# Optimization experiments

Hardware: AMD Instinct MI355X
Metric: run time of the kernel (lower is better)

The kernel has to match this reference:

```python
import jax, jax.numpy as jnp
import numpy as np
import math

DIM = 768
EMB = 768          # dim * num_heads (num_heads=1)
NBLOCKS = 4
M = EMB // 2       # kernel_ratio = 0.5 -> 384 random features
EPS = 1e-8


def monarch_linear(x, w1, w2, b):
    """Monarch (blockdiag butterfly) linear: x [..., n] -> [..., out].
    w1: (k, q, p) with n = k*p ; w2: (l, s, r) with k*q = l*r ; out = l*s."""
    lead = x.shape[:-1]
    k, q, p = w1.shape
    l, s, r = w2.shape
    xf = x.reshape(-1, k, p)                              # (B, k, p)
    o1 = jnp.einsum('bkp,kqp->bkq', xf, w1)               # (B, k, q)
    o1 = o1.transpose(0, 2, 1).reshape(-1, l, r)          # permute then (B, l, r)
    o2 = jnp.einsum('blr,lsr->bls', o1, w2)               # (B, l, s)
    out = o2.transpose(0, 2, 1).reshape(*lead, s * l)     # (B, s, l) flattened
    return out + b


def prm_exp(x, w):
    """FAVOR+ positive random features. x: [b,t,d], w: [m,d]."""
    xd = 0.5 * jnp.sum(x * x, axis=-1, keepdims=True)     # [b,t,1]
    wtx = jnp.einsum('btd,md->btm', x, w)                 # [b,t,m]
    return jnp.exp(wtx - xd) / math.sqrt(M)


def _monarch_params(rng, n_in, n_out, nblocks):
    in_blk = n_in // nblocks
    out_blk = n_out // nblocks
    if n_in < n_out:
        w1 = rng.standard_normal((nblocks, in_blk, in_blk)).astype(np.float32)
        w2 = rng.standard_normal((nblocks, out_blk, in_blk)).astype(np.float32)
    else:
        w1 = rng.standard_normal((nblocks, out_blk, in_blk)).astype(np.float32)
        w2 = rng.standard_normal((nblocks, out_blk, out_blk)).astype(np.float32)
    scale = 1.0 / math.sqrt(n_in)
    b = rng.standard_normal((n_out,)).astype(np.float32) * scale
    return w1 * scale, w2 * scale, b


def setup_inputs() -> dict:
    key = jax.random.key(0)
    x = jax.random.normal(key, (8, 4096, DIM), dtype=jnp.float32)
    rng = np.random.default_rng(0)
    kqv_w1, kqv_w2, kqv_b = _monarch_params(rng, DIM, 3 * EMB, NBLOCKS)
    proj_w1, proj_w2, proj_b = _monarch_params(rng, EMB, EMB, NBLOCKS)
    # orthogonal random-feature matrix, rows orthonormal, scaled by sqrt(m)
    a = rng.standard_normal((EMB, M)).astype(np.float64)
    qmat, _ = np.linalg.qr(a)                             # (EMB, M), cols orthonormal
    w = (qmat.T * math.sqrt(M)).astype(np.float32)        # (M, EMB)
    return {
        'x': x,
        'kqv_w1': jnp.asarray(kqv_w1), 'kqv_w2': jnp.asarray(kqv_w2), 'kqv_b': jnp.asarray(kqv_b),
        'proj_w1': jnp.asarray(proj_w1), 'proj_w2': jnp.asarray(proj_w2), 'proj_b': jnp.asarray(proj_b),
        'w': jnp.asarray(w),
    }


def reference(x, kqv_w1, kqv_w2, kqv_b, proj_w1, proj_w2, proj_b, w):
    kqv = monarch_linear(x, kqv_w1, kqv_w2, kqv_b)        # [b,t,3*EMB]
    k, q, v = jnp.split(kqv, 3, axis=-1)                  # order k,q,v as in torch.split
    kp = prm_exp(k, w)                                    # [b,t,m]
    qp = prm_exp(q, w)                                    # [b,t,m]
    D = jnp.einsum('btm,bm->bt', qp, kp.sum(axis=1))[:, :, None]   # [b,t,1]
    kptv = jnp.einsum('btn,btm->bnm', v, kp)              # [b,EMB,m]
    y = jnp.einsum('btm,bnm->btn', qp, kptv) / (D + EPS)  # [b,t,EMB]
    return monarch_linear(y, proj_w1, proj_w2, proj_b)
```

## Files before the change

### kernel.cpp

```cpp
#include <hip/hip_runtime.h>


#define NTOK   32768
#define RSQRTM 0.05103103630798288f

typedef _Float16 f16;
typedef f16   f16x8 __attribute__((ext_vector_type(8)));
typedef f16   f16x4 __attribute__((ext_vector_type(4)));
typedef short s16x8 __attribute__((ext_vector_type(8)));
typedef float f32x4 __attribute__((ext_vector_type(4)));

typedef const void __attribute__((address_space(1))) gv_t;
typedef void       __attribute__((address_space(3))) lv_t;
#define GLL16(g, l) __builtin_amdgcn_global_load_lds((gv_t*)(g), (lv_t*)(l), 16, 0, 0)

__device__ __forceinline__ float b2f(unsigned short u){
  union{unsigned int i; float f;} v; v.i = ((unsigned int)u)<<16; return v.f;
}
__device__ __forceinline__ unsigned short f2b(float f){
  union{float f; unsigned int i;} v; v.f = f;
  unsigned int x = v.i;
  x += 0x7fffu + ((x>>16)&1u);
  return (unsigned short)(x>>16);
}

template<typename T> struct MfmaOp;
template<> struct MfmaOp<f16> {
  typedef f16x8 frag;
  static __device__ __forceinline__ f32x4 run(frag a, frag b, f32x4 c){
    return __builtin_amdgcn_mfma_f32_16x16x32_f16(a, b, c, 0, 0, 0);
  }
};
template<> struct MfmaOp<short> {
  typedef s16x8 frag;
  static __device__ __forceinline__ f32x4 run(frag a, frag b, f32x4 c){
    return __builtin_amdgcn_mfma_f32_16x16x32_bf16(a, b, c, 0, 0, 0);
  }
};

__global__ void cvt16(const float4* __restrict__ src, f16* __restrict__ dst, int n4){
  const int i = blockIdx.x*256 + threadIdx.x;
  if (i >= n4) return;
  const float4 v = src[i];
  f16x4 h; h[0]=(f16)v.x; h[1]=(f16)v.y; h[2]=(f16)v.z; h[3]=(f16)v.w;
  *reinterpret_cast<f16x4*>(dst + 4*(long)i) = h;
}
__global__ void build_wkqvT(const float* __restrict__ w1, const float* __restrict__ w2,
                            f16* __restrict__ Wt){
  const int idx = blockIdx.x*256 + threadIdx.x;
  const int j = idx / 768, i = idx % 768;
  const int k = i / 192, p = i % 192;
  const int s = j >> 2,  l = j & 3;
  float acc = 0.f;
  #pragma unroll 4
  for(int u=0; u<48; ++u)
    acc += w1[(k*192 + l*48+u)*192 + p] * w2[(l*576+s)*192 + 4*u+k];
  Wt[idx] = (f16)acc;
}
__global__ void build_wprojT(const float* __restrict__ w1, const float* __restrict__ w2,
                             unsigned short* __restrict__ Wt){
  const int idx = blockIdx.x*256 + threadIdx.x;
  const int j = idx / 768, i = idx % 768;
  const int k = i / 192, p = i % 192;
  const int s = j >> 2,  l = j & 3;
  float acc = 0.f;
  #pragma unroll 4
  for(int u=0; u<48; ++u)
    acc += w1[(k*192 + l*48+u)*192 + p] * w2[(l*192+s)*192 + 4*u+k];
  Wt[idx] = f2b(acc);
}
__global__ void reduce_kptv(const float* __restrict__ p32, unsigned short* __restrict__ o){
  const int idx = blockIdx.x*256 + threadIdx.x;
  const int b = idx / 294912, i = idx % 294912;
  const float* base = p32 + (long)b*4*294912 + i;
  o[idx] = f2b(base[0] + base[294912] + base[2*294912] + base[3*294912]);
}

template<typename T, int BM, int BN, int EPI, int SPLIT>
__global__ __launch_bounds__(256)
void mgemm(const T* __restrict__ A, int lda, long aB,
           const T* __restrict__ Bt, int ldb, long bB,
           int K, void* __restrict__ out, int ldo, long outB,
           void* __restrict__ out2,
           const float* __restrict__ aux, long auxB,
           float* __restrict__ aux2){
  constexpr int MT = BM/32, NT = BN/32;
  constexpr int IA = BM/32, IB = BN/32;
  __shared__ T As[BM*64];
  __shared__ T Bs[BN*64];
  typedef typename MfmaOp<T>::frag frag_t;

  const int tid = threadIdx.x, lane = tid & 63, w = tid >> 6;
  const int wm = w >> 1, wn = w & 1;
  const int ln = lane & 15, q = lane >> 4;
  const int bz = blockIdx.z;
  const int batch = bz / SPLIT;
  const int kstart = (bz % SPLIT) * K;
  const long m0 = (long)blockIdx.y * BM;
  const int  n0 = blockIdx.x * BN;
  const T* Ab = A  + (long)batch*aB;
  const T* Bb = Bt + (long)batch*bB;

  f32x4 acc[MT][NT];
  const f32x4 zero = {0.f, 0.f, 0.f, 0.f};
  #pragma unroll
  for(int i=0;i<MT;i++)
    #pragma unroll
    for(int j=0;j<NT;j++) acc[i][j] = zero;

  for (int k0 = kstart; k0 < kstart + K; k0 += 64){
    __syncthreads();
    #pragma unroll
    for (int i = 0; i < IA; ++i){
      const int e = (w*IA + i)*64 + lane;
      const int m = e >> 3, j = (e & 7) ^ (m & 7);
      GLL16(Ab + (m0 + m)*lda + k0 + j*8, As + (size_t)(w*IA + i)*512);
    }
    #pragma unroll
    for (int i = 0; i < IB; ++i){
      const int e = (w*IB + i)*64 + lane;
      const int n = e >> 3, j = (e & 7) ^ (n & 7);
      GLL16(Bb + (long)(n0 + n)*ldb + k0 + j*8, Bs + (size_t)(w*IB + i)*512);
    }
    __syncthreads();

    #pragma unroll
    for (int kk = 0; kk < 2; ++kk){
      frag_t a[MT], b[NT];
      #pragma unroll
      for (int mt=0; mt<MT; ++mt){
        const int r = wm*MT*16 + mt*16 + ln;
        a[mt] = *reinterpret_cast<const frag_t*>(&As[(r*8 + ((kk*4+q) ^ (r&7)))*8]);
      }
      #pragma unroll
      for (int nt=0; nt<NT; ++nt){
        const int r = wn*NT*16 + nt*16 + ln;
        b[nt] = *reinterpret_cast<const frag_t*>(&Bs[(r*8 + ((kk*4+q) ^ (r&7)))*8]);
      }
      #pragma unroll
      for (int mt=0; mt<MT; ++mt)
        #pragma unroll
        for (int nt=0; nt<NT; ++nt)
          acc[mt][nt] = MfmaOp<T>::run(a[mt], b[nt], acc[mt][nt]);
    }
  }

  if constexpr(EPI==1){
    const int b = (int)(m0 >> 12);
    float cs[NT];
    #pragma unroll
    for(int nt=0;nt<NT;nt++) cs[nt]=0.f;
    #pragma unroll
    for (int mt=0; mt<MT; ++mt){
      const long mbase = m0 + wm*MT*16 + mt*16 + q*4;
      float xv[4];
      #pragma unroll
      for(int r=0;r<4;r++) xv[r] = aux[mbase + r];
      #pragma unroll
      for (int nt=0; nt<NT; ++nt){
        const int n = n0 + wn*NT*16 + nt*16 + ln;
        const f32x4 c = acc[mt][nt];
        ushort4 v;
        v.x = f2b(__expf(c[0]-xv[0])*RSQRTM);
        v.y = f2b(__expf(c[1]-xv[1])*RSQRTM);
        v.z = f2b(__expf(c[2]-xv[2])*RSQRTM);
        v.w = f2b(__expf(c[3]-xv[3])*RSQRTM);
        *reinterpret_cast<ushort4*>(&((unsigned short*)out)[(long)n*ldo + mbase]) = v;
        cs[nt] += b2f(v.x)+b2f(v.y)+b2f(v.z)+b2f(v.w);
      }
    }
    #pragma unroll
    for (int nt=0; nt<NT; ++nt){
      cs[nt] += __shfl_xor(cs[nt], 16);
      cs[nt] += __shfl_xor(cs[nt], 32);
      if (lane < 16)
        atomicAdd(&aux2[b*384 + n0 + wn*NT*16 + nt*16 + lane], cs[nt]);
    }
    return;
  }

  #pragma unroll
  for (int mt=0; mt<MT; ++mt){
    const long mbase = m0 + wm*MT*16 + mt*16 + q*4;
    if constexpr(EPI==0){
      const int nw = n0 + wn*NT*16;
      const int part = nw / 768;
      float p[4] = {0.f,0.f,0.f,0.f};
      #pragma unroll
      for (int nt=0; nt<NT; ++nt){
        const int n = nw + nt*16 + ln;
        const f32x4 c = acc[mt][nt];
        const float bv = aux[n];
        if (part < 2){
          f16* KQ = (f16*)out;
          #pragma unroll
          for(int r=0;r<4;r++){
            const f16 h = (f16)(c[r] + bv);
            KQ[(mbase+r)*1536 + n] = h;
            const float hf = (float)h;
            p[r] += hf*hf;
          }
        } else {
          unsigned short* VT = (unsigned short*)out2;
          ushort4 v;
          v.x = f2b(c[0]+bv); v.y = f2b(c[1]+bv); v.z = f2b(c[2]+bv); v.w = f2b(c[3]+bv);
          *reinterpret_cast<ushort4*>(&VT[(long)(n-1536)*32768 + mbase]) = v;
        }
      }
      if (part < 2){
        #pragma unroll
        for(int r=0;r<4;r++){
          #pragma unroll
          for(int mask=1; mask<16; mask<<=1) p[r] += __shfl_xor(p[r], mask);
        }
        if (ln == 0){
          #pragma unroll
          for(int r=0;r<4;r++)
            atomicAdd(&aux2[part*NTOK + mbase + r], 0.5f*p[r]);
        }
      }
    } else if constexpr(EPI==2){
      const int b = (int)(m0 >> 12);
      float xv[4], dp[4] = {0.f,0.f,0.f,0.f};
      #pragma unroll
      for(int r=0;r<4;r++) xv[r] = aux[mbase + r];
      #pragma unroll
      for (int nt=0; nt<NT; ++nt){
        const int n = n0 + wn*NT*16 + nt*16 + ln;
        const f32x4 c = acc[mt][nt];
        const float ksn = aux2[b*384 + n];
        #pragma unroll
        for(int r=0;r<4;r++){
          const unsigned short h = f2b(__expf(c[r]-xv[r])*RSQRTM);
          ((unsigned short*)out)[(mbase+r)*ldo + n] = h;
          dp[r] += b2f(h)*ksn;
        }
      }
      #pragma unroll
      for(int r=0;r<4;r++){
        #pragma unroll
        for(int mask=1; mask<16; mask<<=1) dp[r] += __shfl_xor(dp[r], mask);
      }
      if (ln == 0){
        #pragma unroll
        for(int r=0;r<4;r++)
          atomicAdd(&((float*)out2)[mbase + r], dp[r]);
      }
    } else if constexpr(EPI==3){
      float* o = (float*)out + (long)bz*outB;
      #pragma unroll
      for (int nt=0; nt<NT; ++nt){
        const int n = n0 + wn*NT*16 + nt*16 + ln;
        const f32x4 c = acc[mt][nt];
        #pragma unroll
        for(int r=0;r<4;r++) o[(mbase+r)*ldo + n] = c[r];
      }
    } else if constexpr(EPI==4){
      unsigned short* o = (unsigned short*)out + (long)bz*outB;
      float xv[4];
      #pragma unroll
      for(int r=0;r<4;r++) xv[r] = 1.f/(aux[bz*auxB + mbase + r] + 1e-8f);
      #pragma unroll
      for (int nt=0; nt<NT; ++nt){
        const int n = n0 + wn*NT*16 + nt*16 + ln;
        const f32x4 c = acc[mt][nt];
        #pragma unroll
        for(int r=0;r<4;r++) o[(mbase+r)*ldo + n] = f2b(c[r]*xv[r]);
      }
    } else if constexpr(EPI==5){
      float* o = (float*)out;
      #pragma unroll
      for (int nt=0; nt<NT; ++nt){
        const int n = n0 + wn*NT*16 + nt*16 + ln;
        const f32x4 c = acc[mt][nt];
        const float bv = aux[n];
        #pragma unroll
        for(int r=0;r<4;r++) o[(mbase+r)*ldo + n] = c[r] + bv;
      }
    }
  }
}

extern "C" void kernel_launch(void* const* d_in, const int* in_sizes, int n_in,
                              void* d_out, int out_size, void* d_ws, size_t ws_size,
                              hipStream_t stream){
  (void)in_sizes; (void)n_in; (void)out_size;
  const float* x       = (const float*)d_in[0];
  const float* kqv_w1  = (const float*)d_in[1];
  const float* kqv_w2  = (const float*)d_in[2];
  const float* kqv_b   = (const float*)d_in[3];
  const float* proj_w1 = (const float*)d_in[4];
  const float* proj_w2 = (const float*)d_in[5];
  const float* proj_b  = (const float*)d_in[6];
  const float* w       = (const float*)d_in[7];
  char* ws = (char*)d_ws;

  const size_t o_WkqvT  = 0;
  const size_t o_WprojT = 3538944;
  const size_t o_w16    = 4718592;
  const size_t o_x16    = 5308416;
  const size_t o_KQ     = 55640064;
  const size_t o_VT     = 156303360;
  const size_t o_xd     = 206635008;
  const size_t o_ksum   = 206897152;
  const size_t o_Dv     = 206909440;
  const size_t o_kpT    = 207040512;
  const size_t o_qp     = 232206336;
  const size_t o_kptv32 = 257372160;
  const size_t o_kptv   = 295120896;
  const size_t o_Y      = 299839488;
  const size_t TOTAL    = 350171136;
  if (ws_size < TOTAL) return;

  f16*            WkqvT  = (f16*)(ws + o_WkqvT);
  short*          WprojT = (short*)(ws + o_WprojT);
  f16*            w16    = (f16*)(ws + o_w16);
  f16*            x16    = (f16*)(ws + o_x16);
  f16*            KQ     = (f16*)(ws + o_KQ);
  short*          VT     = (short*)(ws + o_VT);
  float*          xd     = (float*)(ws + o_xd);
  float*          ksum   = (float*)(ws + o_ksum);
  float*          Dv     = (float*)(ws + o_Dv);
  short*          kpT    = (short*)(ws + o_kpT);
  short*          qp     = (short*)(ws + o_qp);
  float*          kptv32 = (float*)(ws + o_kptv32);
  unsigned short* kptv   = (unsigned short*)(ws + o_kptv);
  short*          Y      = (short*)(ws + o_Y);

  hipMemsetAsync(ws + o_xd, 0, 405504, stream);

  cvt16<<<24576, 256, 0, stream>>>((const float4*)x, x16, 6291456);
  cvt16<<<288,   256, 0, stream>>>((const float4*)w, w16, 73728);
  build_wkqvT <<<6912, 256, 0, stream>>>(kqv_w1, kqv_w2, WkqvT);
  build_wprojT<<<2304, 256, 0, stream>>>(proj_w1, proj_w2, (unsigned short*)WprojT);

  mgemm<f16,128,128,0,1><<<dim3(18,256,1), 256, 0, stream>>>(
      x16, 768, 0L, WkqvT, 768, 0L, 768, KQ, 1536, 0L, VT, kqv_b, 0L, xd);

  mgemm<f16,128,128,1,1><<<dim3(3,256,1), 256, 0, stream>>>(
      KQ, 1536, 0L, w16, 768, 0L, 768, kpT, 32768, 0L, nullptr, xd, 0L, ksum);

  mgemm<f16,128,128,2,1><<<dim3(3,256,1), 256, 0, stream>>>(
      KQ + 768, 1536, 0L, w16, 768, 0L, 768, qp, 384, 0L, Dv, xd + NTOK, 0L, ksum);

  mgemm<short,128,128,3,4><<<dim3(3,6,32), 256, 0, stream>>>(
      VT, 32768, 4096L, kpT, 32768, 4096L, 1024, kptv32, 384, 294912L,
      nullptr, nullptr, 0L, nullptr);
  reduce_kptv<<<9216, 256, 0, stream>>>(kptv32, kptv);

  mgemm<short,128,128,4,1><<<dim3(6,32,8), 256, 0, stream>>>(
      qp, 384, 1572864L, (short*)kptv, 384, 294912L, 384, Y, 768, 3145728L,
      nullptr, Dv, 4096L, nullptr);

  mgemm<short,128,128,5,1><<<dim3(6,256,1), 256, 0, stream>>>(
      Y, 768, 0L, WprojT, 768, 0L, 768, d_out, 768, 0L, nullptr, proj_b, 0L, nullptr);
}
```

Baseline: 628.8 us.

## Use 256x256-tile 512-thread GEMM with 4-stage pipeline for KQV and projection

Result: slower. 683.8 us (+8.8%).

```diff
diff --git a/kernel.cpp b/kernel.cpp
--- a/kernel.cpp
+++ b/kernel.cpp
@@ -182,12 +182,174 @@
   #pragma unroll
   for (int mt=0; mt<MT; ++mt){
     const long mbase = m0 + wm*MT*16 + mt*16 + q*4;
-    if constexpr(EPI==0){
-      const int nw = n0 + wn*NT*16;
-      const int part = nw / 768;
+    if constexpr(EPI==2){
+      const int b = (int)(m0 >> 12);
+      float xv[4], dp[4] = {0.f,0.f,0.f,0.f};
+      #pragma unroll
+      for(int r=0;r<4;r++) xv[r] = aux[mbase + r];
+      #pragma unroll
+      for (int nt=0; nt<NT; ++nt){
+        const int n = n0 + wn*NT*16 + nt*16 + ln;
+        const f32x4 c = acc[mt][nt];
+        const float ksn = aux2[b*384 + n];
+        #pragma unroll
+        for(int r=0;r<4;r++){
+          const unsigned short h = f2b(__expf(c[r]-xv[r])*RSQRTM);
+          ((unsigned short*)out)[(mbase+r)*ldo + n] = h;
+          dp[r] += b2f(h)*ksn;
+        }
+      }
+      #pragma unroll
+      for(int r=0;r<4;r++){
+        #pragma unroll
+        for(int mask=1; mask<16; mask<<=1) dp[r] += __shfl_xor(dp[r], mask);
+      }
+      if (ln == 0){
+        #pragma unroll
+        for(int r=0;r<4;r++)
+          atomicAdd(&((float*)out2)[mbase + r], dp[r]);
+      }
+    } else if constexpr(EPI==3){
+      float* o = (float*)out + (long)bz*outB;
+      #pragma unroll
+      for (int nt=0; nt<NT; ++nt){
+        const int n = n0 + wn*NT*16 + nt*16 + ln;
+        const f32x4 c = acc[mt][nt];
+        #pragma unroll
+        for(int r=0;r<4;r++) o[(mbase+r)*ldo + n] = c[r];
+      }
+    } else if constexpr(EPI==4){
+      unsigned short* o = (unsigned short*)out + (long)bz*outB;
+      float xv[4];
+      #pragma unroll
+      for(int r=0;r<4;r++) xv[r] = 1.f/(aux[bz*auxB + mbase + r] + 1e-8f);
+      #pragma unroll
+      for (int nt=0; nt<NT; ++nt){
+        const int n = n0 + wn*NT*16 + nt*16 + ln;
+        const f32x4 c = acc[mt][nt];
+        #pragma unroll
+        for(int r=0;r<4;r++) o[(mbase+r)*ldo + n] = f2b(c[r]*xv[r]);
+      }
+    }
+  }
+}
+
+template<typename T, int EPI, int KTOT>
+__global__ __launch_bounds__(512, 2)
+void mgemm256(const T* __restrict__ A, int lda,
+              const T* __restrict__ Bt, int ldb,
+              void* __restrict__ out, int ldo,
+              void* __restrict__ out2,
+              const float* __restrict__ aux,
+              float* __restrict__ aux2){
+  constexpr int NTIL = KTOT / 32;
+  __shared__ T As[4][8192];
+  __shared__ T Bs[4][8192];
+  typedef typename MfmaOp<T>::frag frag_t;
+
+  const int tid = threadIdx.x, lane = tid & 63, w = tid >> 6;
+  const int wm = w >> 2, wn = w & 3;
+  const int ln = lane & 15, q = lane >> 4;
+
+  const int gx = gridDim.x;
+  const int nwg = gx * (int)gridDim.y;
+  int bid = blockIdx.y * gx + blockIdx.x;
+  bid = (bid & 7) * (nwg >> 3) + (bid >> 3);
+  const int  n0 = (bid % gx) * 256;
+  const long m0 = (long)(bid / gx) * 256;
+
+  const T* ap[2]; const T* bp[2];
+  #pragma unroll
+  for (int i = 0; i < 2; ++i){
+    const int d = (i*512 + tid) * 16;
+    const int l = d ^ (((d >> 7) & 3) << 4);
+    const int row = l >> 6, col = (l & 63) >> 1;
+    ap[i] = A  + (m0 + row) * lda + col;
+    bp[i] = Bt + (long)(n0 + row) * ldb + col;
+  }
+
+  int aoff[8], boff[4];
+  #pragma unroll
+  for (int m = 0; m < 8; ++m){
+    const int r = wm*128 + m*16 + ln;
+    aoff[m] = r*64 + ((q ^ ((r >> 1) & 3)) << 4);
+  }
+  #pragma unroll
+  for (int n = 0; n < 4; ++n){
+    const int r = wn*64 + n*16 + ln;
+    boff[n] = r*64 + ((q ^ ((r >> 1) & 3)) << 4);
+  }
+
+  f32x4 acc[8][4];
+  const f32x4 zero = {0.f,0.f,0.f,0.f};
+  #pragma unroll
+  for (int m=0;m<8;m++)
+    #pragma unroll
+    for (int n=0;n<4;n++) acc[m][n] = zero;
+
+  #pragma unroll
+  for (int t = 0; t < 3; ++t){
+    #pragma unroll
+    for (int i = 0; i < 2; ++i)
+      GLL16(ap[i] + t*32, (T*)As[t] + i*4096 + w*512);
+    #pragma unroll
+    for (int i = 0; i < 2; ++i)
+      GLL16(bp[i] + t*32, (T*)Bs[t] + i*4096 + w*512);
+  }
+
+  for (int t = 0; t < NTIL; ++t){
+    const int s = t & 3;
+    asm volatile("" ::: "memory");
+    __builtin_amdgcn_s_barrier();
+    asm volatile("" ::: "memory");
+    if (t + 3 < NTIL){
+      const int sp = (t+3) & 3;
+      #pragma unroll
+      for (int i = 0; i < 2; ++i)
+        GLL16(ap[i] + (t+3)*32, (T*)As[sp] + i*4096 + w*512);
+      #pragma unroll
+      for (int i = 0; i < 2; ++i)
+        GLL16(bp[i] + (t+3)*32, (T*)Bs[sp] + i*4096 + w*512);
+      asm volatile("s_waitcnt vmcnt(12)" ::: "memory");
+    } else if (t + 2 < NTIL){
+      asm volatile("s_waitcnt vmcnt(8)" ::: "memory");
+    } else if (t + 1 < NTIL){
+      asm volatile("s_waitcnt vmcnt(4)" ::: "memory");
+    } else {
+      asm volatile("s_waitcnt vmcnt(0)" ::: "memory");
+    }
+    __builtin_amdgcn_s_barrier();
+    asm volatile("" ::: "memory");
+
+    const char* SA = (const char*)As[s];
+    const char* SB = (const char*)Bs[s];
+    frag_t b[4];
+    #pragma unroll
+    for (int n=0;n<4;++n) b[n] = *reinterpret_cast<const frag_t*>(SB + boff[n]);
+    #pragma unroll
+    for (int f=0; f<2; ++f){
+      frag_t a[4];
+      #pragma unroll
+      for (int m=0;m<4;++m) a[m] = *reinterpret_cast<const frag_t*>(SA + aoff[f*4+m]);
+      __builtin_amdgcn_s_setprio(1);
+      #pragma unroll
+      for (int m=0;m<4;++m)
+        #pragma unroll
+        for (int n=0;n<4;++n)
+          acc[f*4+m][n] = MfmaOp<T>::run(a[m], b[n], acc[f*4+m][n]);
+      __builtin_amdgcn_s_setprio(0);
+    }
+  }
+
+  if constexpr(EPI==0){
+    const int nw = n0 + wn*64;
+    const int part = nw / 768;
+    #pragma unroll
+    for (int mt=0; mt<8; ++mt){
+      const long mbase = m0 + wm*128 + mt*16 + q*4;
       float p[4] = {0.f,0.f,0.f,0.f};
       #pragma unroll
-      for (int nt=0; nt<NT; ++nt){
+      for (int nt=0; nt<4; ++nt){
         const int n = nw + nt*16 + ln;
         const f32x4 c = acc[mt][nt];
         const float bv = aux[n];
@@ -196,7 +358,7 @@
           #pragma unroll
           for(int r=0;r<4;r++){
             const f16 h = (f16)(c[r] + bv);
-            KQ[(mbase+r)*1536 + n] = h;
+            KQ[(mbase+r)*ldo + n] = h;
             const float hf = (float)h;
             p[r] += hf*hf;
           }
@@ -219,59 +381,15 @@
             atomicAdd(&aux2[part*NTOK + mbase + r], 0.5f*p[r]);
         }
       }
-    } else if constexpr(EPI==2){
-      const int b = (int)(m0 >> 12);
-      float xv[4], dp[4] = {0.f,0.f,0.f,0.f};
-      #pragma unroll
-      for(int r=0;r<4;r++) xv[r] = aux[mbase + r];
-      #pragma unroll
-      for (int nt=0; nt<NT; ++nt){
-        const int n = n0 + wn*NT*16 + nt*16 + ln;
-        const f32x4 c = acc[mt][nt];
-        const float ksn = aux2[b*384 + n];
-        #pragma unroll
-        for(int r=0;r<4;r++){
-          const unsigned short h = f2b(__expf(c[r]-xv[r])*RSQRTM);
-          ((unsigned short*)out)[(mbase+r)*ldo + n] = h;
-          dp[r] += b2f(h)*ksn;
-        }
-      }
-      #pragma unroll
-      for(int r=0;r<4;r++){
-        #pragma unroll
-        for(int mask=1; mask<16; mask<<=1) dp[r] += __shfl_xor(dp[r], mask);
-      }
-      if (ln == 0){
-        #pragma unroll
-        for(int r=0;r<4;r++)
-          atomicAdd(&((float*)out2)[mbase + r], dp[r]);
-      }
-    } else if constexpr(EPI==3){
-      float* o = (float*)out + (long)bz*outB;
-      #pragma unroll
-      for (int nt=0; nt<NT; ++nt){
-        const int n = n0 + wn*NT*16 + nt*16 + ln;
-        const f32x4 c = acc[mt][nt];
-        #pragma unroll
-        for(int r=0;r<4;r++) o[(mbase+r)*ldo + n] = c[r];
-      }
-    } else if constexpr(EPI==4){
-      unsigned short* o = (unsigned short*)out + (long)bz*outB;
-      float xv[4];
-      #pragma unroll
-      for(int r=0;r<4;r++) xv[r] = 1.f/(aux[bz*auxB + mbase + r] + 1e-8f);
-      #pragma unroll
-      for (int nt=0; nt<NT; ++nt){
-        const int n = n0 + wn*NT*16 + nt*16 + ln;
-        const f32x4 c = acc[mt][nt];
-        #pragma unroll
-        for(int r=0;r<4;r++) o[(mbase+r)*ldo + n] = f2b(c[r]*xv[r]);
-      }
-    } else if constexpr(EPI==5){
-      float* o = (float*)out;
-      #pragma unroll
-      for (int nt=0; nt<NT; ++nt){
-        const int n = n0 + wn*NT*16 + nt*16 + ln;
+    }
+  } else {
+    float* o = (float*)out;
+    #pragma unroll
+    for (int mt=0; mt<8; ++mt){
+      const long mbase = m0 + wm*128 + mt*16 + q*4;
+      #pragma unroll
+      for (int nt=0; nt<4; ++nt){
+        const int n = n0 + wn*64 + nt*16 + ln;
         const f32x4 c = acc[mt][nt];
         const float bv = aux[n];
         #pragma unroll
@@ -279,6 +397,7 @@
       }
     }
   }
+  (void)out2; (void)aux2;
 }
 
 extern "C" void kernel_launch(void* const* d_in, const int* in_sizes, int n_in,
@@ -334,8 +453,8 @@
   build_wkqvT <<<6912, 256, 0, stream>>>(kqv_w1, kqv_w2, WkqvT);
   build_wprojT<<<2304, 256, 0, stream>>>(proj_w1, proj_w2, (unsigned short*)WprojT);
 
-  mgemm<f16,128,128,0,1><<<dim3(18,256,1), 256, 0, stream>>>(
-      x16, 768, 0L, WkqvT, 768, 0L, 768, KQ, 1536, 0L, VT, kqv_b, 0L, xd);
+  mgemm256<f16, 0, 768><<<dim3(9,128,1), 512, 0, stream>>>(
+      x16, 768, WkqvT, 768, KQ, 1536, VT, kqv_b, xd);
 
   mgemm<f16,128,128,1,1><<<dim3(3,256,1), 256, 0, stream>>>(
       KQ, 1536, 0L, w16, 768, 0L, 768, kpT, 32768, 0L, nullptr, xd, 0L, ksum);
@@ -352,6 +471,6 @@
       qp, 384, 1572864L, (short*)kptv, 384, 294912L, 384, Y, 768, 3145728L,
       nullptr, Dv, 4096L, nullptr);
 
-  mgemm<short,128,128,5,1><<<dim3(6,256,1), 256, 0, stream>>>(
-      Y, 768, 0L, WprojT, 768, 0L, 768, d_out, 768, 0L, nullptr, proj_b, 0L, nullptr);
-}
+  mgemm256<short, 5, 768><<<dim3(3,128,1), 512, 0, stream>>>(
+      Y, 768, WprojT, 768, d_out, 768, nullptr, proj_b, nullptr);
+}
```

## Fold output projection into per-batch kptv matrix via reassociation

Applied to the files above, without the earlier changes.

New measurement: 613.9 us. 1.02x faster.

```diff
diff --git a/kernel.cpp b/kernel.cpp
--- a/kernel.cpp
+++ b/kernel.cpp
@@ -69,11 +69,24 @@
     acc += w1[(k*192 + l*48+u)*192 + p] * w2[(l*192+s)*192 + 4*u+k];
   Wt[idx] = f2b(acc);
 }
-__global__ void reduce_kptv(const float* __restrict__ p32, unsigned short* __restrict__ o){
-  const int idx = blockIdx.x*256 + threadIdx.x;
-  const int b = idx / 294912, i = idx % 294912;
-  const float* base = p32 + (long)b*4*294912 + i;
-  o[idx] = f2b(base[0] + base[294912] + base[2*294912] + base[3*294912]);
+__global__ void reduce_kptv_t(const float* __restrict__ p32, unsigned short* __restrict__ o){
+  __shared__ float t[64][65];
+  const int b = blockIdx.z, n0 = blockIdx.x*64, m0 = blockIdx.y*64;
+  const int tx = threadIdx.x & 63, ty = threadIdx.x >> 6;
+  const float* base = p32 + (long)b*4*294912;
+  #pragma unroll 4
+  for (int r = 0; r < 16; ++r){
+    const int n = n0 + ty*16 + r;
+    const int idx = n*384 + m0 + tx;
+    t[tx][ty*16+r] = base[idx] + base[294912+idx] + base[2*294912+idx] + base[3*294912+idx];
+  }
+  __syncthreads();
+  unsigned short* ob = o + (long)b*294912;
+  #pragma unroll 4
+  for (int r = 0; r < 16; ++r){
+    const int m = m0 + ty*16 + r;
+    ob[(long)m*768 + n0 + tx] = f2b(t[ty*16+r][tx]);
+  }
 }
 
 template<typename T, int BM, int BN, int EPI, int SPLIT>
@@ -255,8 +268,17 @@
         #pragma unroll
         for(int r=0;r<4;r++) o[(mbase+r)*ldo + n] = c[r];
       }
-    } else if constexpr(EPI==4){
+    } else if constexpr(EPI==6){
       unsigned short* o = (unsigned short*)out + (long)bz*outB;
+      #pragma unroll
+      for (int nt=0; nt<NT; ++nt){
+        const int n = n0 + wn*NT*16 + nt*16 + ln;
+        const f32x4 c = acc[mt][nt];
+        #pragma unroll
+        for(int r=0;r<4;r++) o[(mbase+r)*ldo + n] = f2b(c[r]);
+      }
+    } else if constexpr(EPI==7){
+      float* o = (float*)out + (long)bz*outB;
       float xv[4];
       #pragma unroll
       for(int r=0;r<4;r++) xv[r] = 1.f/(aux[bz*auxB + mbase + r] + 1e-8f);
@@ -264,18 +286,9 @@
       for (int nt=0; nt<NT; ++nt){
         const int n = n0 + wn*NT*16 + nt*16 + ln;
         const f32x4 c = acc[mt][nt];
-        #pragma unroll
-        for(int r=0;r<4;r++) o[(mbase+r)*ldo + n] = f2b(c[r]*xv[r]);
-      }
-    } else if constexpr(EPI==5){
-      float* o = (float*)out;
-      #pragma unroll
-      for (int nt=0; nt<NT; ++nt){
-        const int n = n0 + wn*NT*16 + nt*16 + ln;
-        const f32x4 c = acc[mt][nt];
-        const float bv = aux[n];
-        #pragma unroll
-        for(int r=0;r<4;r++) o[(mbase+r)*ldo + n] = c[r] + bv;
+        const float bv = aux2[n];
+        #pragma unroll
+        for(int r=0;r<4;r++) o[(mbase+r)*ldo + n] = c[r]*xv[r] + bv;
       }
     }
   }
@@ -307,9 +320,9 @@
   const size_t o_kpT    = 207040512;
   const size_t o_qp     = 232206336;
   const size_t o_kptv32 = 257372160;
-  const size_t o_kptv   = 295120896;
-  const size_t o_Y      = 299839488;
-  const size_t TOTAL    = 350171136;
+  const size_t o_kptvT  = 295120896;
+  const size_t o_Z      = 299839488;
+  const size_t TOTAL    = 304558080;
   if (ws_size < TOTAL) return;
 
   f16*            WkqvT  = (f16*)(ws + o_WkqvT);
@@ -324,8 +337,8 @@
   short*          kpT    = (short*)(ws + o_kpT);
   short*          qp     = (short*)(ws + o_qp);
   float*          kptv32 = (float*)(ws + o_kptv32);
-  unsigned short* kptv   = (unsigned short*)(ws + o_kptv);
-  short*          Y      = (short*)(ws + o_Y);
+  unsigned short* kptvT  = (unsigned short*)(ws + o_kptvT);
+  short*          Z      = (short*)(ws + o_Z);
 
   hipMemsetAsync(ws + o_xd, 0, 405504, stream);
 
@@ -346,12 +359,14 @@
   mgemm<short,128,128,3,4><<<dim3(3,6,32), 256, 0, stream>>>(
       VT, 32768, 4096L, kpT, 32768, 4096L, 1024, kptv32, 384, 294912L,
       nullptr, nullptr, 0L, nullptr);
-  reduce_kptv<<<9216, 256, 0, stream>>>(kptv32, kptv);
-
-  mgemm<short,128,128,4,1><<<dim3(6,32,8), 256, 0, stream>>>(
-      qp, 384, 1572864L, (short*)kptv, 384, 294912L, 384, Y, 768, 3145728L,
-      nullptr, Dv, 4096L, nullptr);
-
-  mgemm<short,128,128,5,1><<<dim3(6,256,1), 256, 0, stream>>>(
-      Y, 768, 0L, WprojT, 768, 0L, 768, d_out, 768, 0L, nullptr, proj_b, 0L, nullptr);
-}
+
+  reduce_kptv_t<<<dim3(12,6,8), 256, 0, stream>>>(kptv32, kptvT);
+
+  mgemm<short,128,128,6,1><<<dim3(3,6,8), 256, 0, stream>>>(
+      WprojT, 768, 0L, (short*)kptvT, 768, 294912L, 768, Z, 384, 294912L,
+      nullptr, nullptr, 0L, nullptr);
+
+  mgemm<short,128,128,7,1><<<dim3(6,32,8), 256, 0, stream>>>(
+      qp, 384, 1572864L, Z, 384, 294912L, 384, d_out, 768, 3145728L,
+      nullptr, Dv, 4096L, (float*)proj_b);
+}
```
